# Kernel optimization log

Hardware: AMD Instinct MI355X
Metric: run time of the kernel (lower is better)

The kernel has to match this reference:

```python
import jax, jax.numpy as jnp
import numpy as np

BLOCK_SIZE = 256
NEG = -10000.0  # matches the module's additive mask constant (not -inf)

def setup_inputs() -> dict:
    key = jax.random.key(0)
    qkv = jax.random.normal(key, (4, 4096, 192), dtype=jnp.float32)
    return {"qkv": qkv}

def reference(qkv):
    B, S, dm = qkv.shape
    d = dm // 3
    q, k, v = qkv[..., :d], qkv[..., d:2*d], qkv[..., 2*d:]
    scale = 1.0 / jnp.sqrt(jnp.asarray(d, dtype=qkv.dtype))
    scores = jnp.einsum('bqd,bkd->bqk', q, k * scale)  # [B,S,S]
    i = jnp.arange(S)[:, None]
    j = jnp.arange(S)[None, :]
    # allowed: i - block_size <= j <= i ; else additive -10000 (as in torch code)
    mask = jnp.where((j <= i) & (j >= i - BLOCK_SIZE), 0.0, NEG).astype(scores.dtype)
    attn = jax.nn.softmax(scores + mask[None, :, :], axis=-1)
    return jnp.einsum('bqk,bkd->bqd', attn, v)
```

## Files before the change

### kernel.cpp

```cpp
#include <hip/hip_runtime.h>
#include <hip/hip_bf16.h>


#define LOG2E 1.4426950408889634f

typedef __attribute__((ext_vector_type(8))) short  frag;
typedef __attribute__((ext_vector_type(4))) float  f32x4;

static __device__ inline short f2bf(float x) {
    __hip_bfloat16 h = __float2bfloat16(x);
    return __builtin_bit_cast(short, h);
}

#define DPPF(x, ctrl) __builtin_bit_cast(float, \
    __builtin_amdgcn_mov_dpp(__builtin_bit_cast(int, (x)), (ctrl), 0xF, 0xF, true))

static __device__ inline float red16_max(float x) {
    x = fmaxf(x, DPPF(x, 0xB1));
    x = fmaxf(x, DPPF(x, 0x4E));
    x = fmaxf(x, DPPF(x, 0x141));
    x = fmaxf(x, DPPF(x, 0x140));
    return x;
}
static __device__ inline float red16_sum(float x) {
    x += DPPF(x, 0xB1);
    x += DPPF(x, 0x4E);
    x += DPPF(x, 0x141);
    x += DPPF(x, 0x140);
    return x;
}

#define LSTR 72
#define PSTR 40
#define OSTR 65

__global__ __launch_bounds__(512, 2) void swa_mfma2(const float* __restrict__ qkv,
                                                    float* __restrict__ out)
{
    __shared__ short Qs[64 * LSTR];
    __shared__ short Ks[64 * LSTR];
    __shared__ short Vt[64 * LSTR];
    __shared__ short Pw[8][16 * PSTR];
    __shared__ float Om[4][16 * OSTR];
    __shared__ float2 mlbuf[4][16];

    const int b    = blockIdx.y;
    const int q0   = blockIdx.x * 64;
    const int t    = threadIdx.x;
    const int w    = t >> 6;
    const int s    = w & 3;
    const int g    = w >> 2;
    const int lane = t & 63;
    const int cl   = lane & 15;
    const int quad = lane >> 4;
    const int ql   = 4 * quad;

    const float4* qkv4 = (const float4*)qkv;
    const int r_st = t >> 3;
    const int c8   = t & 7;

    {
        const size_t base = (size_t)(b * 4096 + q0 + r_st) * 48;
        #pragma unroll
        for (int i = 0; i < 2; ++i) {
            float4 v = qkv4[base + c8 + 8 * i];
            short4 s4 = { f2bf(v.x * 0.125f), f2bf(v.y * 0.125f),
                          f2bf(v.z * 0.125f), f2bf(v.w * 0.125f) };
            *(short4*)&Qs[r_st * LSTR + 4 * (c8 + 8 * i)] = s4;
        }
    }

    const int c0 = (q0 >= 256) ? 0 : (4 - (q0 >> 6));

    float4 preK[2], preV[2];
    {
        const int kb = q0 - 256 + 64 * c0;
        const size_t base = (size_t)(b * 4096 + kb + r_st) * 48;
        #pragma unroll
        for (int i = 0; i < 2; ++i) {
            preK[i] = qkv4[base + 16 + c8 + 8 * i];
            preV[i] = qkv4[base + 32 + c8 + 8 * i];
        }
    }

    __syncthreads();
    const frag qf0 = *(const frag*)&Qs[(16 * s + cl) * LSTR + 8 * quad];
    const frag qf1 = *(const frag*)&Qs[(16 * s + cl) * LSTR + 32 + 8 * quad];

    float m[4], l[4];
    f32x4 oacc[4];
    #pragma unroll
    for (int r = 0; r < 4; ++r) { m[r] = -1e30f; l[r] = 0.f; }
    #pragma unroll
    for (int n4 = 0; n4 < 4; ++n4) oacc[n4] = (f32x4){0.f, 0.f, 0.f, 0.f};

    for (int c = c0; c < 5; ++c) {
        __syncthreads();

        #pragma unroll
        for (int i = 0; i < 2; ++i) {
            short4 k4 = { f2bf(preK[i].x), f2bf(preK[i].y),
                          f2bf(preK[i].z), f2bf(preK[i].w) };
            *(short4*)&Ks[r_st * LSTR + 4 * (c8 + 8 * i)] = k4;
            const int d0 = 4 * (c8 + 8 * i);
            Vt[(d0 + 0) * LSTR + r_st] = f2bf(preV[i].x);
            Vt[(d0 + 1) * LSTR + r_st] = f2bf(preV[i].y);
            Vt[(d0 + 2) * LSTR + r_st] = f2bf(preV[i].z);
            Vt[(d0 + 3) * LSTR + r_st] = f2bf(preV[i].w);
        }
        __syncthreads();

        if (c < 4) {
            const int kb = q0 - 256 + 64 * (c + 1);
            const size_t base = (size_t)(b * 4096 + kb + r_st) * 48;
            #pragma unroll
            for (int i = 0; i < 2; ++i) {
                preK[i] = qkv4[base + 16 + c8 + 8 * i];
                preV[i] = qkv4[base + 32 + c8 + 8 * i];
            }
        }

        f32x4 sc[2];
        #pragma unroll
        for (int u = 0; u < 2; ++u) {
            const int t4 = 2 * g + u;
            sc[u] = (f32x4){0.f, 0.f, 0.f, 0.f};
            const frag kf0 = *(const frag*)&Ks[(16 * t4 + cl) * LSTR + 8 * quad];
            const frag kf1 = *(const frag*)&Ks[(16 * t4 + cl) * LSTR + 32 + 8 * quad];
            sc[u] = __builtin_amdgcn_mfma_f32_16x16x32_bf16(qf0, kf0, sc[u], 0, 0, 0);
            sc[u] = __builtin_amdgcn_mfma_f32_16x16x32_bf16(qf1, kf1, sc[u], 0, 0, 0);
        }

        if (c == 4) {
            #pragma unroll
            for (int u = 0; u < 2; ++u) {
                const int t4 = 2 * g + u;
                #pragma unroll
                for (int r = 0; r < 4; ++r)
                    if (16 * s + ql + r < 16 * t4 + cl) sc[u][r] = -1e30f;
            }
        } else if (c == 0) {
            #pragma unroll
            for (int u = 0; u < 2; ++u) {
                const int t4 = 2 * g + u;
                #pragma unroll
                for (int r = 0; r < 4; ++r)
                    if (16 * s + ql + r > 16 * t4 + cl) sc[u][r] = -1e30f;
            }
        }

        #pragma unroll
        for (int r = 0; r < 4; ++r) {
            float mx = red16_max(fmaxf(sc[0][r], sc[1][r]));
            const float mnew  = fmaxf(m[r], mx);
            const float alpha = __builtin_amdgcn_exp2f((m[r] - mnew) * LOG2E);
            m[r] = mnew;
            float sum = 0.f;
            #pragma unroll
            for (int u = 0; u < 2; ++u) {
                float p = (sc[u][r] <= -1e29f)
                            ? 0.f
                            : __builtin_amdgcn_exp2f((sc[u][r] - mnew) * LOG2E);
                Pw[w][(ql + r) * PSTR + 16 * u + cl] = f2bf(p);
                sum += p;
            }
            l[r] = l[r] * alpha + red16_sum(sum);
            #pragma unroll
            for (int n4 = 0; n4 < 4; ++n4) oacc[n4][r] *= alpha;
        }

        const frag pf = *(const frag*)&Pw[w][cl * PSTR + 8 * quad];
        #pragma unroll
        for (int n4 = 0; n4 < 4; ++n4) {
            const frag vf = *(const frag*)&Vt[(16 * n4 + cl) * LSTR + 32 * g + 8 * quad];
            oacc[n4] = __builtin_amdgcn_mfma_f32_16x16x32_bf16(pf, vf, oacc[n4], 0, 0, 0);
        }
    }

    if (g == 1) {
        #pragma unroll
        for (int n4 = 0; n4 < 4; ++n4)
            #pragma unroll
            for (int r = 0; r < 4; ++r)
                Om[s][(ql + r) * OSTR + 16 * n4 + cl] = oacc[n4][r];
        if (cl == 0)
            #pragma unroll
            for (int r = 0; r < 4; ++r)
                mlbuf[s][ql + r] = make_float2(m[r], l[r]);
    }
    __syncthreads();
    if (g == 0) {
        #pragma unroll
        for (int r = 0; r < 4; ++r) {
            const float2 ml1 = mlbuf[s][ql + r];
            const float M  = fmaxf(m[r], ml1.x);
            const float a0 = __builtin_amdgcn_exp2f((m[r]  - M) * LOG2E);
            const float a1 = __builtin_amdgcn_exp2f((ml1.x - M) * LOG2E);
            const float L  = l[r] * a0 + ml1.y * a1;
            const float inv = 1.0f / L;
            const size_t row = (size_t)(b * 4096 + q0 + 16 * s + ql + r) * 64;
            #pragma unroll
            for (int n4 = 0; n4 < 4; ++n4) {
                const float o1 = Om[s][(ql + r) * OSTR + 16 * n4 + cl];
                out[row + 16 * n4 + cl] = (oacc[n4][r] * a0 + o1 * a1) * inv;
            }
        }
    }
}

extern "C" void kernel_launch(void* const* d_in, const int* in_sizes, int n_in,
                              void* d_out, int out_size, void* d_ws, size_t ws_size,
                              hipStream_t stream) {
    const float* qkv = (const float*)d_in[0];
    float* out = (float*)d_out;
    dim3 grid(64, 4);
    dim3 block(512);
    hipLaunchKernelGGL(swa_mfma2, grid, block, 0, stream, qkv, out);
}
```

Baseline: 67.31 us.

## Stage all K/V window chunks into LDS upfront and drop per-chunk barriers

Instead of double-buffering one 64-key chunk at a time through registers with two barriers per iteration, the kernel now loads and converts all five K/V chunks of the sliding window into enlarged shared-memory buffers before computing. The compute loop is fully unrolled and indexes into the chunk offset, with no synchronisation inside it. This aims to issue all global loads concurrently and remove per-chunk barrier stalls. The cost is a much larger LDS footprint, which may limit resident blocks per CU.

Result: slower. 70.30 us (+4.4%).

```diff
diff --git a/kernel.cpp b/kernel.cpp
--- a/kernel.cpp
+++ b/kernel.cpp
@@ -31,15 +31,16 @@
 }
 
 #define LSTR 72
+#define VSTR 328
 #define PSTR 40
 #define OSTR 65
 
-__global__ __launch_bounds__(512, 2) void swa_mfma2(const float* __restrict__ qkv,
+__global__ __launch_bounds__(512, 2) void swa_mfma3(const float* __restrict__ qkv,
                                                     float* __restrict__ out)
 {
     __shared__ short Qs[64 * LSTR];
-    __shared__ short Ks[64 * LSTR];
-    __shared__ short Vt[64 * LSTR];
+    __shared__ short Ks[320 * LSTR];
+    __shared__ short Vt[64 * VSTR];
     __shared__ short Pw[8][16 * PSTR];
     __shared__ float Om[4][16 * OSTR];
     __shared__ float2 mlbuf[4][16];
@@ -59,6 +60,8 @@
     const int r_st = t >> 3;
     const int c8   = t & 7;
 
+    const int c0 = (q0 >= 256) ? 0 : (4 - (q0 >> 6));
+
     {
         const size_t base = (size_t)(b * 4096 + q0 + r_st) * 48;
         #pragma unroll
@@ -70,20 +73,27 @@
         }
     }
 
-    const int c0 = (q0 >= 256) ? 0 : (4 - (q0 >> 6));
-
-    float4 preK[2], preV[2];
-    {
-        const int kb = q0 - 256 + 64 * c0;
-        const size_t base = (size_t)(b * 4096 + kb + r_st) * 48;
+    const int kbase = b * 4096 + q0 - 256;
+    #pragma unroll
+    for (int c = 0; c < 5; ++c) {
+        if (c < c0) continue;
+        const size_t base = (size_t)(kbase + 64 * c + r_st) * 48;
         #pragma unroll
         for (int i = 0; i < 2; ++i) {
-            preK[i] = qkv4[base + 16 + c8 + 8 * i];
-            preV[i] = qkv4[base + 32 + c8 + 8 * i];
+            float4 kv = qkv4[base + 16 + c8 + 8 * i];
+            float4 vv = qkv4[base + 32 + c8 + 8 * i];
+            short4 k4 = { f2bf(kv.x), f2bf(kv.y), f2bf(kv.z), f2bf(kv.w) };
+            *(short4*)&Ks[(64 * c + r_st) * LSTR + 4 * (c8 + 8 * i)] = k4;
+            const int d0 = 4 * (c8 + 8 * i);
+            Vt[(d0 + 0) * VSTR + 64 * c + r_st] = f2bf(vv.x);
+            Vt[(d0 + 1) * VSTR + 64 * c + r_st] = f2bf(vv.y);
+            Vt[(d0 + 2) * VSTR + 64 * c + r_st] = f2bf(vv.z);
+            Vt[(d0 + 3) * VSTR + 64 * c + r_st] = f2bf(vv.w);
         }
     }
 
     __syncthreads();
+
     const frag qf0 = *(const frag*)&Qs[(16 * s + cl) * LSTR + 8 * quad];
     const frag qf1 = *(const frag*)&Qs[(16 * s + cl) * LSTR + 32 + 8 * quad];
 
@@ -94,39 +104,18 @@
     #pragma unroll
     for (int n4 = 0; n4 < 4; ++n4) oacc[n4] = (f32x4){0.f, 0.f, 0.f, 0.f};
 
-    for (int c = c0; c < 5; ++c) {
-        __syncthreads();
-
-        #pragma unroll
-        for (int i = 0; i < 2; ++i) {
-            short4 k4 = { f2bf(preK[i].x), f2bf(preK[i].y),
-                          f2bf(preK[i].z), f2bf(preK[i].w) };
-            *(short4*)&Ks[r_st * LSTR + 4 * (c8 + 8 * i)] = k4;
-            const int d0 = 4 * (c8 + 8 * i);
-            Vt[(d0 + 0) * LSTR + r_st] = f2bf(preV[i].x);
-            Vt[(d0 + 1) * LSTR + r_st] = f2bf(preV[i].y);
-            Vt[(d0 + 2) * LSTR + r_st] = f2bf(preV[i].z);
-            Vt[(d0 + 3) * LSTR + r_st] = f2bf(preV[i].w);
-        }
-        __syncthreads();
-
-        if (c < 4) {
-            const int kb = q0 - 256 + 64 * (c + 1);
-            const size_t base = (size_t)(b * 4096 + kb + r_st) * 48;
-            #pragma unroll
-            for (int i = 0; i < 2; ++i) {
-                preK[i] = qkv4[base + 16 + c8 + 8 * i];
-                preV[i] = qkv4[base + 32 + c8 + 8 * i];
-            }
-        }
+    #pragma unroll
+    for (int c = 0; c < 5; ++c) {
+        if (c < c0) continue;
 
         f32x4 sc[2];
         #pragma unroll
         for (int u = 0; u < 2; ++u) {
             const int t4 = 2 * g + u;
+            const int krow = 64 * c + 16 * t4;
             sc[u] = (f32x4){0.f, 0.f, 0.f, 0.f};
-            const frag kf0 = *(const frag*)&Ks[(16 * t4 + cl) * LSTR + 8 * quad];
-            const frag kf1 = *(const frag*)&Ks[(16 * t4 + cl) * LSTR + 32 + 8 * quad];
+            const frag kf0 = *(const frag*)&Ks[(krow + cl) * LSTR + 8 * quad];
+            const frag kf1 = *(const frag*)&Ks[(krow + cl) * LSTR + 32 + 8 * quad];
             sc[u] = __builtin_amdgcn_mfma_f32_16x16x32_bf16(qf0, kf0, sc[u], 0, 0, 0);
             sc[u] = __builtin_amdgcn_mfma_f32_16x16x32_bf16(qf1, kf1, sc[u], 0, 0, 0);
         }
@@ -172,7 +161,7 @@
         const frag pf = *(const frag*)&Pw[w][cl * PSTR + 8 * quad];
         #pragma unroll
         for (int n4 = 0; n4 < 4; ++n4) {
-            const frag vf = *(const frag*)&Vt[(16 * n4 + cl) * LSTR + 32 * g + 8 * quad];
+            const frag vf = *(const frag*)&Vt[(16 * n4 + cl) * VSTR + 64 * c + 32 * g + 8 * quad];
             oacc[n4] = __builtin_amdgcn_mfma_f32_16x16x32_bf16(pf, vf, oacc[n4], 0, 0, 0);
         }
     }
@@ -215,5 +204,5 @@
     float* out = (float*)d_out;
     dim3 grid(64, 4);
     dim3 block(512);
-    hipLaunchKernelGGL(swa_mfma2, grid, block, 0, stream, qkv, out);
-}
+    hipLaunchKernelGGL(swa_mfma3, grid, block, 0, stream, qkv, out);
+}
```

## Split key tile across four wave groups with 1024-thread blocks

Applied to the files above, without the earlier changes.

Doubles the block to 16 waves so each of four wave groups handles 16 keys of every 64-key tile, instead of two groups handling 32 keys each. Each group keeps its own online-softmax state, and group 0 merges the other three partial results through shared memory at the end. This is meant to raise parallelism and latency hiding, since the grid has only 256 blocks. In exchange, each PV MFMA now runs half-empty with zero-padded fragments, there are more reductions and barrier participants per tile, and the final merge step costs more.

Measured after the change: 70.81 us. 1.05x slower.

```diff
diff --git a/kernel.cpp b/kernel.cpp
--- a/kernel.cpp
+++ b/kernel.cpp
@@ -30,19 +30,20 @@
     return x;
 }
 
-#define LSTR 72
-#define PSTR 40
+#define KSTR 72
+#define VSTR 65
+#define PSTR 20
 #define OSTR 65
 
-__global__ __launch_bounds__(512, 2) void swa_mfma2(const float* __restrict__ qkv,
-                                                    float* __restrict__ out)
+__global__ __launch_bounds__(1024, 4) void swa_mfma6(const float* __restrict__ qkv,
+                                                     float* __restrict__ out)
 {
-    __shared__ short Qs[64 * LSTR];
-    __shared__ short Ks[64 * LSTR];
-    __shared__ short Vt[64 * LSTR];
-    __shared__ short Pw[8][16 * PSTR];
-    __shared__ float Om[4][16 * OSTR];
-    __shared__ float2 mlbuf[4][16];
+    __shared__ short Qs[64 * KSTR];
+    __shared__ short Ks[64 * KSTR];
+    __shared__ short Vt[64 * VSTR + 16];
+    __shared__ short Pw[16][16 * PSTR];
+    __shared__ float Om[4][3][16 * OSTR];
+    __shared__ float2 mlbuf[4][3][16];
 
     const int b    = blockIdx.y;
     const int q0   = blockIdx.x * 64;
@@ -56,36 +57,30 @@
     const int ql   = 4 * quad;
 
     const float4* qkv4 = (const float4*)qkv;
-    const int r_st = t >> 3;
-    const int c8   = t & 7;
+    const int r_st = t >> 4;
+    const int c16  = t & 15;
+
+    const int c0 = (q0 >= 256) ? 0 : (4 - (q0 >> 6));
 
     {
         const size_t base = (size_t)(b * 4096 + q0 + r_st) * 48;
-        #pragma unroll
-        for (int i = 0; i < 2; ++i) {
-            float4 v = qkv4[base + c8 + 8 * i];
-            short4 s4 = { f2bf(v.x * 0.125f), f2bf(v.y * 0.125f),
-                          f2bf(v.z * 0.125f), f2bf(v.w * 0.125f) };
-            *(short4*)&Qs[r_st * LSTR + 4 * (c8 + 8 * i)] = s4;
-        }
-    }
-
-    const int c0 = (q0 >= 256) ? 0 : (4 - (q0 >> 6));
-
-    float4 preK[2], preV[2];
+        float4 v = qkv4[base + c16];
+        short4 s4 = { f2bf(v.x * 0.125f), f2bf(v.y * 0.125f),
+                      f2bf(v.z * 0.125f), f2bf(v.w * 0.125f) };
+        *(short4*)&Qs[r_st * KSTR + 4 * c16] = s4;
+    }
+
+    float4 pK, pV;
     {
         const int kb = q0 - 256 + 64 * c0;
         const size_t base = (size_t)(b * 4096 + kb + r_st) * 48;
-        #pragma unroll
-        for (int i = 0; i < 2; ++i) {
-            preK[i] = qkv4[base + 16 + c8 + 8 * i];
-            preV[i] = qkv4[base + 32 + c8 + 8 * i];
-        }
+        pK = qkv4[base + 16 + c16];
+        pV = qkv4[base + 32 + c16];
     }
 
     __syncthreads();
-    const frag qf0 = *(const frag*)&Qs[(16 * s + cl) * LSTR + 8 * quad];
-    const frag qf1 = *(const frag*)&Qs[(16 * s + cl) * LSTR + 32 + 8 * quad];
+    const frag qf0 = *(const frag*)&Qs[(16 * s + cl) * KSTR + 8 * quad];
+    const frag qf1 = *(const frag*)&Qs[(16 * s + cl) * KSTR + 32 + 8 * quad];
 
     float m[4], l[4];
     f32x4 oacc[4];
@@ -97,113 +92,106 @@
     for (int c = c0; c < 5; ++c) {
         __syncthreads();
 
-        #pragma unroll
-        for (int i = 0; i < 2; ++i) {
-            short4 k4 = { f2bf(preK[i].x), f2bf(preK[i].y),
-                          f2bf(preK[i].z), f2bf(preK[i].w) };
-            *(short4*)&Ks[r_st * LSTR + 4 * (c8 + 8 * i)] = k4;
-            const int d0 = 4 * (c8 + 8 * i);
-            Vt[(d0 + 0) * LSTR + r_st] = f2bf(preV[i].x);
-            Vt[(d0 + 1) * LSTR + r_st] = f2bf(preV[i].y);
-            Vt[(d0 + 2) * LSTR + r_st] = f2bf(preV[i].z);
-            Vt[(d0 + 3) * LSTR + r_st] = f2bf(preV[i].w);
+        {
+            short4 k4 = { f2bf(pK.x), f2bf(pK.y), f2bf(pK.z), f2bf(pK.w) };
+            *(short4*)&Ks[r_st * KSTR + 4 * c16] = k4;
+            const int d0 = 4 * c16;
+            Vt[(d0 + 0) * VSTR + r_st] = f2bf(pV.x);
+            Vt[(d0 + 1) * VSTR + r_st] = f2bf(pV.y);
+            Vt[(d0 + 2) * VSTR + r_st] = f2bf(pV.z);
+            Vt[(d0 + 3) * VSTR + r_st] = f2bf(pV.w);
         }
         __syncthreads();
 
         if (c < 4) {
             const int kb = q0 - 256 + 64 * (c + 1);
             const size_t base = (size_t)(b * 4096 + kb + r_st) * 48;
-            #pragma unroll
-            for (int i = 0; i < 2; ++i) {
-                preK[i] = qkv4[base + 16 + c8 + 8 * i];
-                preV[i] = qkv4[base + 32 + c8 + 8 * i];
-            }
-        }
-
-        f32x4 sc[2];
-        #pragma unroll
-        for (int u = 0; u < 2; ++u) {
-            const int t4 = 2 * g + u;
-            sc[u] = (f32x4){0.f, 0.f, 0.f, 0.f};
-            const frag kf0 = *(const frag*)&Ks[(16 * t4 + cl) * LSTR + 8 * quad];
-            const frag kf1 = *(const frag*)&Ks[(16 * t4 + cl) * LSTR + 32 + 8 * quad];
-            sc[u] = __builtin_amdgcn_mfma_f32_16x16x32_bf16(qf0, kf0, sc[u], 0, 0, 0);
-            sc[u] = __builtin_amdgcn_mfma_f32_16x16x32_bf16(qf1, kf1, sc[u], 0, 0, 0);
+            pK = qkv4[base + 16 + c16];
+            pV = qkv4[base + 32 + c16];
+        }
+
+        f32x4 sc = (f32x4){0.f, 0.f, 0.f, 0.f};
+        {
+            const frag kf0 = *(const frag*)&Ks[(16 * g + cl) * KSTR + 8 * quad];
+            const frag kf1 = *(const frag*)&Ks[(16 * g + cl) * KSTR + 32 + 8 * quad];
+            sc = __builtin_amdgcn_mfma_f32_16x16x32_bf16(qf0, kf0, sc, 0, 0, 0);
+            sc = __builtin_amdgcn_mfma_f32_16x16x32_bf16(qf1, kf1, sc, 0, 0, 0);
         }
 
         if (c == 4) {
             #pragma unroll
-            for (int u = 0; u < 2; ++u) {
-                const int t4 = 2 * g + u;
-                #pragma unroll
-                for (int r = 0; r < 4; ++r)
-                    if (16 * s + ql + r < 16 * t4 + cl) sc[u][r] = -1e30f;
-            }
+            for (int r = 0; r < 4; ++r)
+                if (16 * s + ql + r < 16 * g + cl) sc[r] = -1e30f;
         } else if (c == 0) {
             #pragma unroll
-            for (int u = 0; u < 2; ++u) {
-                const int t4 = 2 * g + u;
-                #pragma unroll
-                for (int r = 0; r < 4; ++r)
-                    if (16 * s + ql + r > 16 * t4 + cl) sc[u][r] = -1e30f;
-            }
+            for (int r = 0; r < 4; ++r)
+                if (16 * s + ql + r > 16 * g + cl) sc[r] = -1e30f;
         }
 
         #pragma unroll
         for (int r = 0; r < 4; ++r) {
-            float mx = red16_max(fmaxf(sc[0][r], sc[1][r]));
+            const float mx = red16_max(sc[r]);
             const float mnew  = fmaxf(m[r], mx);
             const float alpha = __builtin_amdgcn_exp2f((m[r] - mnew) * LOG2E);
             m[r] = mnew;
-            float sum = 0.f;
-            #pragma unroll
-            for (int u = 0; u < 2; ++u) {
-                float p = (sc[u][r] <= -1e29f)
-                            ? 0.f
-                            : __builtin_amdgcn_exp2f((sc[u][r] - mnew) * LOG2E);
-                Pw[w][(ql + r) * PSTR + 16 * u + cl] = f2bf(p);
-                sum += p;
-            }
-            l[r] = l[r] * alpha + red16_sum(sum);
+            const float p = (sc[r] <= -1e29f)
+                              ? 0.f
+                              : __builtin_amdgcn_exp2f((sc[r] - mnew) * LOG2E);
+            Pw[w][(ql + r) * PSTR + cl] = f2bf(p);
+            l[r] = l[r] * alpha + red16_sum(p);
             #pragma unroll
             for (int n4 = 0; n4 < 4; ++n4) oacc[n4][r] *= alpha;
         }
 
-        const frag pf = *(const frag*)&Pw[w][cl * PSTR + 8 * quad];
+        frag pf = (frag){0, 0, 0, 0, 0, 0, 0, 0};
+        if (quad < 2) pf = *(const frag*)&Pw[w][cl * PSTR + 8 * quad];
         #pragma unroll
         for (int n4 = 0; n4 < 4; ++n4) {
-            const frag vf = *(const frag*)&Vt[(16 * n4 + cl) * LSTR + 32 * g + 8 * quad];
+            frag vf = (frag){0, 0, 0, 0, 0, 0, 0, 0};
+            if (quad < 2)
+                vf = *(const frag*)&Vt[(16 * n4 + cl) * VSTR + 16 * g + 8 * quad];
             oacc[n4] = __builtin_amdgcn_mfma_f32_16x16x32_bf16(pf, vf, oacc[n4], 0, 0, 0);
         }
     }
 
-    if (g == 1) {
+    if (g != 0) {
         #pragma unroll
         for (int n4 = 0; n4 < 4; ++n4)
             #pragma unroll
             for (int r = 0; r < 4; ++r)
-                Om[s][(ql + r) * OSTR + 16 * n4 + cl] = oacc[n4][r];
+                Om[s][g - 1][(ql + r) * OSTR + 16 * n4 + cl] = oacc[n4][r];
         if (cl == 0)
             #pragma unroll
             for (int r = 0; r < 4; ++r)
-                mlbuf[s][ql + r] = make_float2(m[r], l[r]);
+                mlbuf[s][g - 1][ql + r] = make_float2(m[r], l[r]);
     }
     __syncthreads();
     if (g == 0) {
         #pragma unroll
         for (int r = 0; r < 4; ++r) {
-            const float2 ml1 = mlbuf[s][ql + r];
-            const float M  = fmaxf(m[r], ml1.x);
-            const float a0 = __builtin_amdgcn_exp2f((m[r]  - M) * LOG2E);
-            const float a1 = __builtin_amdgcn_exp2f((ml1.x - M) * LOG2E);
-            const float L  = l[r] * a0 + ml1.y * a1;
+            float M = m[r];
+            float L = l[r];
+            float acc[4];
+            #pragma unroll
+            for (int n4 = 0; n4 < 4; ++n4) acc[n4] = oacc[n4][r];
+            #pragma unroll
+            for (int p = 0; p < 3; ++p) {
+                const float2 ml = mlbuf[s][p][ql + r];
+                const float Mn = fmaxf(M, ml.x);
+                const float a0 = __builtin_amdgcn_exp2f((M    - Mn) * LOG2E);
+                const float a1 = __builtin_amdgcn_exp2f((ml.x - Mn) * LOG2E);
+                L = L * a0 + ml.y * a1;
+                #pragma unroll
+                for (int n4 = 0; n4 < 4; ++n4)
+                    acc[n4] = acc[n4] * a0
+                            + Om[s][p][(ql + r) * OSTR + 16 * n4 + cl] * a1;
+                M = Mn;
+            }
             const float inv = 1.0f / L;
             const size_t row = (size_t)(b * 4096 + q0 + 16 * s + ql + r) * 64;
             #pragma unroll
-            for (int n4 = 0; n4 < 4; ++n4) {
-                const float o1 = Om[s][(ql + r) * OSTR + 16 * n4 + cl];
-                out[row + 16 * n4 + cl] = (oacc[n4][r] * a0 + o1 * a1) * inv;
-            }
+            for (int n4 = 0; n4 < 4; ++n4)
+                out[row + 16 * n4 + cl] = acc[n4] * inv;
         }
     }
 }
@@ -214,6 +202,6 @@
     const float* qkv = (const float*)d_in[0];
     float* out = (float*)d_out;
     dim3 grid(64, 4);
-    dim3 block(512);
-    hipLaunchKernelGGL(swa_mfma2, grid, block, 0, stream, qkv, out);
-}
+    dim3 block(1024);
+    hipLaunchKernelGGL(swa_mfma6, grid, block, 0, stream, qkv, out);
+}
```

## Double-buffer K/V tiles in shared memory to drop one barrier per iteration

Applied to the files above, without the earlier changes.

K and V^T shared tiles become ping-pong buffers. The next tile is converted and staged into the alternate buffer while the current one is consumed, and the global prefetch runs two tiles ahead. This leaves one barrier per iteration instead of two and overlaps staging with the MFMA and softmax work. The cost is double the K/V LDS footprint and extra registers for the deeper prefetch, which may affect occupancy at 2 blocks of 512 threads.

Measured after the change: 69.99 us. 4.0% more time.

```diff
diff --git a/kernel.cpp b/kernel.cpp
--- a/kernel.cpp
+++ b/kernel.cpp
@@ -34,12 +34,12 @@
 #define PSTR 40
 #define OSTR 65
 
-__global__ __launch_bounds__(512, 2) void swa_mfma2(const float* __restrict__ qkv,
+__global__ __launch_bounds__(512, 2) void swa_mfma7(const float* __restrict__ qkv,
                                                     float* __restrict__ out)
 {
     __shared__ short Qs[64 * LSTR];
-    __shared__ short Ks[64 * LSTR];
-    __shared__ short Vt[64 * LSTR];
+    __shared__ short Ks[2][64 * LSTR];
+    __shared__ short Vt[2][64 * LSTR];
     __shared__ short Pw[8][16 * PSTR];
     __shared__ float Om[4][16 * OSTR];
     __shared__ float2 mlbuf[4][16];
@@ -59,6 +59,8 @@
     const int r_st = t >> 3;
     const int c8   = t & 7;
 
+    const int c0 = (q0 >= 256) ? 0 : (4 - (q0 >> 6));
+
     {
         const size_t base = (size_t)(b * 4096 + q0 + r_st) * 48;
         #pragma unroll
@@ -70,18 +72,33 @@
         }
     }
 
-    const int c0 = (q0 >= 256) ? 0 : (4 - (q0 >> 6));
-
     float4 preK[2], preV[2];
-    {
-        const int kb = q0 - 256 + 64 * c0;
+    auto fetch = [&](int c) {
+        const int kb = q0 - 256 + 64 * c;
         const size_t base = (size_t)(b * 4096 + kb + r_st) * 48;
         #pragma unroll
         for (int i = 0; i < 2; ++i) {
             preK[i] = qkv4[base + 16 + c8 + 8 * i];
             preV[i] = qkv4[base + 32 + c8 + 8 * i];
         }
-    }
+    };
+    auto stage = [&](int p) {
+        #pragma unroll
+        for (int i = 0; i < 2; ++i) {
+            short4 k4 = { f2bf(preK[i].x), f2bf(preK[i].y),
+                          f2bf(preK[i].z), f2bf(preK[i].w) };
+            *(short4*)&Ks[p][r_st * LSTR + 4 * (c8 + 8 * i)] = k4;
+            const int d0 = 4 * (c8 + 8 * i);
+            Vt[p][(d0 + 0) * LSTR + r_st] = f2bf(preV[i].x);
+            Vt[p][(d0 + 1) * LSTR + r_st] = f2bf(preV[i].y);
+            Vt[p][(d0 + 2) * LSTR + r_st] = f2bf(preV[i].z);
+            Vt[p][(d0 + 3) * LSTR + r_st] = f2bf(preV[i].w);
+        }
+    };
+
+    fetch(c0);
+    stage(0);
+    if (c0 < 4) fetch(c0 + 1);
 
     __syncthreads();
     const frag qf0 = *(const frag*)&Qs[(16 * s + cl) * LSTR + 8 * quad];
@@ -95,38 +112,18 @@
     for (int n4 = 0; n4 < 4; ++n4) oacc[n4] = (f32x4){0.f, 0.f, 0.f, 0.f};
 
     for (int c = c0; c < 5; ++c) {
-        __syncthreads();
-
-        #pragma unroll
-        for (int i = 0; i < 2; ++i) {
-            short4 k4 = { f2bf(preK[i].x), f2bf(preK[i].y),
-                          f2bf(preK[i].z), f2bf(preK[i].w) };
-            *(short4*)&Ks[r_st * LSTR + 4 * (c8 + 8 * i)] = k4;
-            const int d0 = 4 * (c8 + 8 * i);
-            Vt[(d0 + 0) * LSTR + r_st] = f2bf(preV[i].x);
-            Vt[(d0 + 1) * LSTR + r_st] = f2bf(preV[i].y);
-            Vt[(d0 + 2) * LSTR + r_st] = f2bf(preV[i].z);
-            Vt[(d0 + 3) * LSTR + r_st] = f2bf(preV[i].w);
-        }
-        __syncthreads();
-
-        if (c < 4) {
-            const int kb = q0 - 256 + 64 * (c + 1);
-            const size_t base = (size_t)(b * 4096 + kb + r_st) * 48;
-            #pragma unroll
-            for (int i = 0; i < 2; ++i) {
-                preK[i] = qkv4[base + 16 + c8 + 8 * i];
-                preV[i] = qkv4[base + 32 + c8 + 8 * i];
-            }
-        }
+        const int p = (c - c0) & 1;
+
+        if (c < 4) stage(p ^ 1);
+        if (c < 3) fetch(c + 2);
 
         f32x4 sc[2];
         #pragma unroll
         for (int u = 0; u < 2; ++u) {
             const int t4 = 2 * g + u;
             sc[u] = (f32x4){0.f, 0.f, 0.f, 0.f};
-            const frag kf0 = *(const frag*)&Ks[(16 * t4 + cl) * LSTR + 8 * quad];
-            const frag kf1 = *(const frag*)&Ks[(16 * t4 + cl) * LSTR + 32 + 8 * quad];
+            const frag kf0 = *(const frag*)&Ks[p][(16 * t4 + cl) * LSTR + 8 * quad];
+            const frag kf1 = *(const frag*)&Ks[p][(16 * t4 + cl) * LSTR + 32 + 8 * quad];
             sc[u] = __builtin_amdgcn_mfma_f32_16x16x32_bf16(qf0, kf0, sc[u], 0, 0, 0);
             sc[u] = __builtin_amdgcn_mfma_f32_16x16x32_bf16(qf1, kf1, sc[u], 0, 0, 0);
         }
@@ -158,11 +155,11 @@
             float sum = 0.f;
             #pragma unroll
             for (int u = 0; u < 2; ++u) {
-                float p = (sc[u][r] <= -1e29f)
+                float pv = (sc[u][r] <= -1e29f)
                             ? 0.f
                             : __builtin_amdgcn_exp2f((sc[u][r] - mnew) * LOG2E);
-                Pw[w][(ql + r) * PSTR + 16 * u + cl] = f2bf(p);
-                sum += p;
+                Pw[w][(ql + r) * PSTR + 16 * u + cl] = f2bf(pv);
+                sum += pv;
             }
             l[r] = l[r] * alpha + red16_sum(sum);
             #pragma unroll
@@ -172,9 +169,11 @@
         const frag pf = *(const frag*)&Pw[w][cl * PSTR + 8 * quad];
         #pragma unroll
         for (int n4 = 0; n4 < 4; ++n4) {
-            const frag vf = *(const frag*)&Vt[(16 * n4 + cl) * LSTR + 32 * g + 8 * quad];
+            const frag vf = *(const frag*)&Vt[p][(16 * n4 + cl) * LSTR + 32 * g + 8 * quad];
             oacc[n4] = __builtin_amdgcn_mfma_f32_16x16x32_bf16(pf, vf, oacc[n4], 0, 0, 0);
         }
+
+        __syncthreads();
     }
 
     if (g == 1) {
@@ -215,5 +214,5 @@
     float* out = (float*)d_out;
     dim3 grid(64, 4);
     dim3 block(512);
-    hipLaunchKernelGGL(swa_mfma2, grid, block, 0, stream, qkv, out);
-}
+    hipLaunchKernelGGL(swa_mfma7, grid, block, 0, stream, qkv, out);
+}
```
